# Performance work log

Measured on AMD Instinct MI355X. Metric: run time of the kernel, lower is better.

The kernel has to match this reference:

```python
import jax, jax.numpy as jnp
import numpy as np

N_NODES = 100000
N_EDGES = 1200000
D = 64          # node_feat_size
G_FEAT = 128    # graph_feat_size
N_GRAPHS = 256
N_TASKS = 1


def setup_inputs() -> dict:
    key = jax.random.key(0)
    ks = jax.random.split(key, 12)
    node_feats = jax.random.normal(ks[0], (N_NODES, D), dtype=jnp.float32)
    edge_feats = jax.random.normal(ks[1], (N_EDGES, 8), dtype=jnp.float32)
    src = jax.random.randint(ks[2], (N_EDGES,), 0, N_NODES, dtype=jnp.int64 if jax.config.read('jax_enable_x64') else jnp.int32)
    dst = jax.random.randint(ks[3], (N_EDGES,), 0, N_NODES, dtype=src.dtype)
    graph_ids = jnp.sort(jax.random.randint(ks[4], (N_NODES,), 0, N_GRAPHS, dtype=src.dtype))
    s = 1.0 / np.sqrt(D)
    W_gcn = jax.random.uniform(ks[5], (D, D), minval=-s, maxval=s, dtype=jnp.float32)
    b_gcn = jnp.zeros((D,), jnp.float32)
    W_res = jax.random.uniform(ks[6], (D, D), minval=-s, maxval=s, dtype=jnp.float32)
    b_res = jnp.zeros((D,), jnp.float32)
    W_in = jax.random.uniform(ks[7], (D, D), minval=-s, maxval=s, dtype=jnp.float32)
    b_in = jnp.zeros((D,), jnp.float32)
    W_out = jax.random.uniform(ks[8], (D, G_FEAT), minval=-s, maxval=s, dtype=jnp.float32)
    b_out = jnp.zeros((G_FEAT,), jnp.float32)
    sp = 1.0 / np.sqrt(G_FEAT)
    W_pred = jax.random.uniform(ks[9], (G_FEAT, N_TASKS), minval=-sp, maxval=sp, dtype=jnp.float32)
    b_pred = jnp.zeros((N_TASKS,), jnp.float32)
    return dict(node_feats=node_feats, edge_feats=edge_feats, src=src, dst=dst,
                graph_ids=graph_ids, W_gcn=W_gcn, b_gcn=b_gcn, W_res=W_res, b_res=b_res,
                W_in=W_in, b_in=b_in, W_out=W_out, b_out=b_out, W_pred=W_pred, b_pred=b_pred)


def reference(node_feats, edge_feats, src, dst, graph_ids,
              W_gcn, b_gcn, W_res, b_res, W_in, b_in, W_out, b_out, W_pred, b_pred):
    # --- GCNLayer (GraphConv norm='none', activation=relu, residual=True) ---
    # message passing: copy src features, sum at dst (no normalization)
    agg = jax.ops.segment_sum(node_feats[src], dst, num_segments=N_NODES)  # [N, D]
    h = jax.nn.relu(agg @ W_gcn + b_gcn)                                   # graph_conv output
    h = h + jax.nn.relu(node_feats @ W_res + b_res)                        # residual branch
    # --- MLPNodeReadout (mode='sum') ---
    h = jax.nn.relu(h @ W_in + b_in)      # [N, D]
    h = h @ W_out + b_out                 # [N, G_FEAT]
    g_feats = jax.ops.segment_sum(h, graph_ids, num_segments=N_GRAPHS)  # [G, G_FEAT]
    # --- predict ---
    out = (g_feats @ W_pred + b_pred).reshape(-1)  # [G * n_tasks]
    return out
```

## Files before the change

### kernel.cpp

```cpp
#include <hip/hip_runtime.h>

typedef __attribute__((ext_vector_type(8))) __bf16 bf16x8;
typedef __attribute__((ext_vector_type(4))) float f32x4;

union Frag { unsigned short u[8]; bf16x8 b; };

__device__ __forceinline__ unsigned short rne_bf16(float x) {
    unsigned int u = __float_as_uint(x);
    return (unsigned short)((u + 0x7fffu + ((u >> 16) & 1u)) >> 16);
}
__device__ __forceinline__ float bf16_to_f(unsigned short h) {
    return __uint_as_float(((unsigned int)h) << 16);
}

#define MFMA16 __builtin_amdgcn_mfma_f32_16x16x32_bf16
#define SBSH 10
#define SBN 1024
#define SBCAP 13056
#define BINCHUNK 4096
#define NWFRAG (3 * 2 * 2 * 4 * 64 * 8)

__global__ __launch_bounds__(256) void prepbinA_kernel(
    const float* __restrict__ nf, const int* __restrict__ src,
    const int* __restrict__ dst,
    const float* __restrict__ Wg, const float* __restrict__ Wr,
    const float* __restrict__ Wi, const float* __restrict__ Wo,
    const float* __restrict__ bo, const float* __restrict__ Wp,
    const float* __restrict__ bp,
    unsigned short* __restrict__ nfb, unsigned short* __restrict__ wfrag,
    float* __restrict__ wfold, float* __restrict__ c0, float* __restrict__ out,
    int* __restrict__ gcursor, int* __restrict__ binned,
    int nBin, int nE, int nbS, int out_size, int nNodes) {
    __shared__ int lhist[128], lbase[128], lpos[128];
    const int t = threadIdx.x;
    if ((int)blockIdx.x < nBin) {
        for (int i = t; i < nbS; i += 256) { lhist[i] = 0; lpos[i] = 0; }
        __syncthreads();
        const int e0 = blockIdx.x * BINCHUNK;
        const int e1 = min(e0 + BINCHUNK, nE);
        for (int e = e0 + t; e < e1; e += 256)
            atomicAdd(&lhist[dst[e] >> SBSH], 1);
        __syncthreads();
        for (int i = t; i < nbS; i += 256) {
            int c = lhist[i];
            lbase[i] = c ? atomicAdd(&gcursor[i], c) : 0;
        }
        __syncthreads();
        for (int e = e0 + t; e < e1; e += 256) {
            int d = dst[e];
            int sb = d >> SBSH;
            int p = atomicAdd(&lpos[sb], 1);
            int gp = lbase[sb] + p;
            if (gp < SBCAP) binned[sb * SBCAP + gp] = (src[e] << SBSH) | (d & (SBN - 1));
        }
    }
    const int tp = (int)blockIdx.x * 256 + t;
    const int nth = (int)gridDim.x * 256;
    const float4* nf4 = (const float4*)nf;
    ushort4* nfb4 = (ushort4*)nfb;
    const int nQ = nNodes * 16;
    for (int i = tp; i < nQ; i += nth) {
        float4 v = nf4[i];
        ushort4 o;
        o.x = rne_bf16(v.x); o.y = rne_bf16(v.y);
        o.z = rne_bf16(v.z); o.w = rne_bf16(v.w);
        nfb4[i] = o;
    }
    const float* Ws[3] = {Wg, Wr, Wi};
    for (int idx = tp; idx < NWFRAG; idx += nth) {
        int j = idx & 7, lane = (idx >> 3) & 63, nt = (idx >> 9) & 3;
        int kt = (idx >> 11) & 1, part = (idx >> 12) & 1, mat = idx >> 13;
        int k = kt * 32 + ((lane >> 4) << 3) + j;
        int n = nt * 16 + (lane & 15);
        float w = Ws[mat][k * 64 + n];
        unsigned short hi = rne_bf16(w);
        wfrag[idx] = (part == 0) ? hi : rne_bf16(w - bf16_to_f(hi));
    }
    if (tp < 64) {
        float s = 0.f;
        for (int j = 0; j < 128; ++j) s += Wo[tp * 128 + j] * Wp[j];
        wfold[tp] = s;
    }
    if (tp == 0) {
        float s = 0.f;
        for (int j = 0; j < 128; ++j) s += bo[j] * Wp[j];
        c0[0] = s;
    }
    if (tp < out_size) out[tp] = bp[0];
}

__global__ __launch_bounds__(1024) void segB_kernel(
    int* __restrict__ binned, const int* __restrict__ gcursor,
    int2* __restrict__ nodeTab, int nNodes) {
    __shared__ int eL[SBCAP];
    __shared__ int deg[SBN], sc[SBN], cur[SBN];
    const int b = blockIdx.x, t = threadIdx.x;
    const int cnt = min(gcursor[b], SBCAP);
    deg[t] = 0;
    __syncthreads();
    for (int i = t; i < cnt; i += 1024) {
        int p = binned[b * SBCAP + i];
        eL[i] = p;
        atomicAdd(&deg[p & (SBN - 1)], 1);
    }
    __syncthreads();
    sc[t] = deg[t];
    __syncthreads();
    #pragma unroll
    for (int s = 1; s < SBN; s <<= 1) {
        int v = (t >= s) ? sc[t - s] : 0;
        __syncthreads();
        sc[t] += v;
        __syncthreads();
    }
    {
        int excl = sc[t] - deg[t];
        cur[t] = excl;
        int node = b * SBN + t;
        if (node < nNodes) nodeTab[node] = make_int2(b * SBCAP + excl, deg[t]);
    }
    __syncthreads();
    for (int i = t; i < cnt; i += 1024) {
        int p = eL[i];
        int pos = atomicAdd(&cur[p & (SBN - 1)], 1);
        binned[b * SBCAP + pos] = p >> SBSH;
    }
}

__global__ __launch_bounds__(256) void gather_kernel(
    const unsigned short* __restrict__ nfb, const int2* __restrict__ nodeTab,
    const int* __restrict__ srcs, unsigned short* __restrict__ aggb, int nNodes) {
    int wid = blockIdx.x * 4 + (threadIdx.x >> 6);
    if (wid >= nNodes) return;
    int lane = threadIdx.x & 63;
    int half = lane >> 5;
    int cp = lane & 31;
    int2 sd = nodeTab[wid];
    int base = sd.x, d = sd.y;
    const ushort2* nfb2 = (const ushort2*)nfb;
    float ax = 0.f, ay = 0.f;
    int k = half;
    for (; k + 8 <= d; k += 8) {
        int s0 = srcs[base + k],     s1 = srcs[base + k + 2];
        int s2 = srcs[base + k + 4], s3 = srcs[base + k + 6];
        ushort2 v0 = nfb2[(long)s0 * 32 + cp];
        ushort2 v1 = nfb2[(long)s1 * 32 + cp];
        ushort2 v2 = nfb2[(long)s2 * 32 + cp];
        ushort2 v3 = nfb2[(long)s3 * 32 + cp];
        ax += (bf16_to_f(v0.x) + bf16_to_f(v1.x)) + (bf16_to_f(v2.x) + bf16_to_f(v3.x));
        ay += (bf16_to_f(v0.y) + bf16_to_f(v1.y)) + (bf16_to_f(v2.y) + bf16_to_f(v3.y));
    }
    for (; k < d; k += 2) {
        int s = srcs[base + k];
        ushort2 v = nfb2[(long)s * 32 + cp];
        ax += bf16_to_f(v.x); ay += bf16_to_f(v.y);
    }
    ax += __shfl_xor(ax, 32, 64);
    ay += __shfl_xor(ay, 32, 64);
    if (half == 0) {
        ushort2 o; o.x = rne_bf16(ax); o.y = rne_bf16(ay);
        ((ushort2*)aggb)[(long)wid * 32 + cp] = o;
    }
}

__global__ __launch_bounds__(256) void mlp_kernel(
    const unsigned short* __restrict__ aggb, const unsigned short* __restrict__ nfb,
    const int* __restrict__ gids, const unsigned short* __restrict__ wfrag,
    const float* __restrict__ bg, const float* __restrict__ br,
    const float* __restrict__ bi, const float* __restrict__ wfold,
    const float* __restrict__ c0p, float* __restrict__ out, int nTiles) {
    __shared__ float hs_all[4][32 * 68];
    const int wave = threadIdx.x >> 6, lane = threadIdx.x & 63;
    const int wid = blockIdx.x * 4 + wave;
    if (wid >= nTiles) return;
    float* hs = hs_all[wave];
    const int base = wid * 32;
    const int mrow = lane & 15, quad = lane >> 4;

    Frag aA[2][2], aN[2][2];
    #pragma unroll
    for (int rt = 0; rt < 2; ++rt) {
        const unsigned short* rowA = aggb + (long)(base + rt * 16 + mrow) * 64;
        const unsigned short* rowN = nfb  + (long)(base + rt * 16 + mrow) * 64;
        #pragma unroll
        for (int kt = 0; kt < 2; ++kt) {
            aA[rt][kt].b = *(const bf16x8*)(rowA + kt * 32 + quad * 8);
            aN[rt][kt].b = *(const bf16x8*)(rowN + kt * 32 + quad * 8);
        }
    }

    const unsigned short* wl0 = wfrag + lane * 8;
    auto WF = [&](int mat, int part, int kt, int nt) -> bf16x8 {
        return *(const bf16x8*)(wl0 + (size_t)((((mat * 2 + part) * 2 + kt) * 4 + nt) * 64) * 8);
    };

    f32x4 accA[2][4], accR[2][4];
    #pragma unroll
    for (int rt = 0; rt < 2; ++rt)
        #pragma unroll
        for (int nt = 0; nt < 4; ++nt) {
            accA[rt][nt] = (f32x4){0.f, 0.f, 0.f, 0.f};
            accR[rt][nt] = (f32x4){0.f, 0.f, 0.f, 0.f};
        }
    #pragma unroll
    for (int nt = 0; nt < 4; ++nt)
        #pragma unroll
        for (int kt = 0; kt < 2; ++kt) {
            bf16x8 gh = WF(0, 0, kt, nt), gl = WF(0, 1, kt, nt);
            bf16x8 rh = WF(1, 0, kt, nt), rl = WF(1, 1, kt, nt);
            #pragma unroll
            for (int rt = 0; rt < 2; ++rt) {
                accA[rt][nt] = MFMA16(aA[rt][kt].b, gh, accA[rt][nt], 0, 0, 0);
                accA[rt][nt] = MFMA16(aA[rt][kt].b, gl, accA[rt][nt], 0, 0, 0);
                accR[rt][nt] = MFMA16(aN[rt][kt].b, rh, accR[rt][nt], 0, 0, 0);
                accR[rt][nt] = MFMA16(aN[rt][kt].b, rl, accR[rt][nt], 0, 0, 0);
            }
        }

    #pragma unroll
    for (int nt = 0; nt < 4; ++nt) {
        float bgv = bg[nt * 16 + mrow], brv = br[nt * 16 + mrow];
        #pragma unroll
        for (int rt = 0; rt < 2; ++rt)
            #pragma unroll
            for (int r = 0; r < 4; ++r) {
                float h = fmaxf(accA[rt][nt][r] + bgv, 0.f)
                        + fmaxf(accR[rt][nt][r] + brv, 0.f);
                hs[(rt * 16 + quad * 4 + r) * 68 + nt * 16 + mrow] = h;
            }
    }
    __builtin_amdgcn_wave_barrier();

    Frag aH[2][2];
    #pragma unroll
    for (int rt = 0; rt < 2; ++rt)
        #pragma unroll
        for (int kt = 0; kt < 2; ++kt) {
            const float* hp = hs + (rt * 16 + mrow) * 68 + kt * 32 + quad * 8;
            float4 v0 = *(const float4*)hp;
            float4 v1 = *(const float4*)(hp + 4);
            aH[rt][kt].u[0] = rne_bf16(v0.x); aH[rt][kt].u[1] = rne_bf16(v0.y);
            aH[rt][kt].u[2] = rne_bf16(v0.z); aH[rt][kt].u[3] = rne_bf16(v0.w);
            aH[rt][kt].u[4] = rne_bf16(v1.x); aH[rt][kt].u[5] = rne_bf16(v1.y);
            aH[rt][kt].u[6] = rne_bf16(v1.z); aH[rt][kt].u[7] = rne_bf16(v1.w);
        }
    f32x4 accH[2][4];
    #pragma unroll
    for (int rt = 0; rt < 2; ++rt)
        #pragma unroll
        for (int nt = 0; nt < 4; ++nt)
            accH[rt][nt] = (f32x4){0.f, 0.f, 0.f, 0.f};
    #pragma unroll
    for (int nt = 0; nt < 4; ++nt)
        #pragma unroll
        for (int kt = 0; kt < 2; ++kt) {
            bf16x8 ih = WF(2, 0, kt, nt), il = WF(2, 1, kt, nt);
            #pragma unroll
            for (int rt = 0; rt < 2; ++rt) {
                accH[rt][nt] = MFMA16(aH[rt][kt].b, ih, accH[rt][nt], 0, 0, 0);
                accH[rt][nt] = MFMA16(aH[rt][kt].b, il, accH[rt][nt], 0, 0, 0);
            }
        }

    float p[2][4];
    #pragma unroll
    for (int rt = 0; rt < 2; ++rt)
        #pragma unroll
        for (int r = 0; r < 4; ++r) p[rt][r] = 0.f;
    #pragma unroll
    for (int nt = 0; nt < 4; ++nt) {
        float biv = bi[nt * 16 + mrow], wfv = wfold[nt * 16 + mrow];
        #pragma unroll
        for (int rt = 0; rt < 2; ++rt)
            #pragma unroll
            for (int r = 0; r < 4; ++r)
                p[rt][r] += fmaxf(accH[rt][nt][r] + biv, 0.f) * wfv;
    }
    #pragma unroll
    for (int m = 1; m <= 8; m <<= 1)
        #pragma unroll
        for (int rt = 0; rt < 2; ++rt)
            #pragma unroll
            for (int r = 0; r < 4; ++r)
                p[rt][r] += __shfl_xor(p[rt][r], m, 64);
    const float c0 = c0p[0];
    #pragma unroll
    for (int rt = 0; rt < 2; ++rt)
        #pragma unroll
        for (int r = 0; r < 4; ++r) p[rt][r] += c0;

    int gself = gids[base + (lane & 31)];
    int g0 = __shfl(gself, 0, 64);
    if (__all(gself == g0)) {
        float pv = 0.f;
        if (mrow == 0) {
            #pragma unroll
            for (int rt = 0; rt < 2; ++rt)
                #pragma unroll
                for (int r = 0; r < 4; ++r) pv += p[rt][r];
        }
        pv += __shfl_xor(pv, 16, 64);
        pv += __shfl_xor(pv, 32, 64);
        if (lane == 0) atomicAdd(out + g0, pv);
    } else if (mrow == 0) {
        #pragma unroll
        for (int rt = 0; rt < 2; ++rt)
            #pragma unroll
            for (int r = 0; r < 4; ++r)
                atomicAdd(out + gids[base + rt * 16 + quad * 4 + r], p[rt][r]);
    }
}

extern "C" void kernel_launch(void* const* d_in, const int* in_sizes, int n_in,
                              void* d_out, int out_size, void* d_ws, size_t ws_size,
                              hipStream_t stream) {
    const float* node_feats = (const float*)d_in[0];
    const int* src  = (const int*)d_in[2];
    const int* dst  = (const int*)d_in[3];
    const int* gids = (const int*)d_in[4];
    const float* Wg = (const float*)d_in[5];
    const float* bg = (const float*)d_in[6];
    const float* Wr = (const float*)d_in[7];
    const float* br = (const float*)d_in[8];
    const float* Wi = (const float*)d_in[9];
    const float* bi = (const float*)d_in[10];
    const float* Wo = (const float*)d_in[11];
    const float* bo = (const float*)d_in[12];
    const float* Wp = (const float*)d_in[13];
    const float* bp = (const float*)d_in[14];
    float* out = (float*)d_out;

    const int nNodes = in_sizes[0] / 64;
    const int nE = in_sizes[2];
    const int nbS = (nNodes + SBN - 1) / SBN;

    int* gcursor = (int*)d_ws;
    int* binned  = gcursor + 128;
    int2* nodeTab = (int2*)(binned + (size_t)nbS * SBCAP);
    unsigned short* nfb  = (unsigned short*)(nodeTab + nNodes);
    unsigned short* aggb = nfb + (size_t)nNodes * 64;
    unsigned short* wfrag = aggb + (size_t)nNodes * 64;
    float* wfold = (float*)(wfrag + NWFRAG);
    float* c0 = wfold + 64;

    hipMemsetAsync(gcursor, 0, 128 * sizeof(int), stream);

    const int nBin = (nE + BINCHUNK - 1) / BINCHUNK;
    prepbinA_kernel<<<nBin + 512, 256, 0, stream>>>(
        node_feats, src, dst, Wg, Wr, Wi, Wo, bo, Wp, bp,
        nfb, wfrag, wfold, c0, out, gcursor, binned,
        nBin, nE, nbS, out_size, nNodes);

    segB_kernel<<<nbS, 1024, 0, stream>>>(binned, gcursor, nodeTab, nNodes);

    gather_kernel<<<(nNodes + 3) / 4, 256, 0, stream>>>(nfb, nodeTab, binned, aggb, nNodes);

    const int nTiles = (nNodes + 31) / 32;
    mlp_kernel<<<(nTiles + 3) / 4, 256, 0, stream>>>(aggb, nfb, gids, wfrag,
        bg, br, bi, wfold, c0, out, nTiles);
}
```

Baseline: 231.7 us.

## Fuse all stages into one cooperative persistent kernel with grid syncs

```diff
diff --git a/kernel.cpp b/kernel.cpp
--- a/kernel.cpp
+++ b/kernel.cpp
@@ -1,4 +1,6 @@
 #include <hip/hip_runtime.h>
+#include <hip/hip_cooperative_groups.h>
+namespace cg = cooperative_groups;
 
 typedef __attribute__((ext_vector_type(8))) __bf16 bf16x8;
 typedef __attribute__((ext_vector_type(4))) float f32x4;
@@ -19,6 +21,309 @@
 #define SBCAP 13056
 #define BINCHUNK 4096
 #define NWFRAG (3 * 2 * 2 * 4 * 64 * 8)
+
+__global__ __launch_bounds__(256, 4) void mega_kernel(
+    const float* __restrict__ nf, const int* __restrict__ src,
+    const int* __restrict__ dst, const int* __restrict__ gids,
+    const float* __restrict__ Wg, const float* __restrict__ bg,
+    const float* __restrict__ Wr, const float* __restrict__ br,
+    const float* __restrict__ Wi, const float* __restrict__ bi,
+    const float* __restrict__ Wo, const float* __restrict__ bo,
+    const float* __restrict__ Wp, const float* __restrict__ bp,
+    int* __restrict__ gcursor, int* __restrict__ binned,
+    int* __restrict__ srcs2, int2* __restrict__ nodeTab,
+    unsigned short* __restrict__ nfb, unsigned short* __restrict__ aggb,
+    unsigned short* __restrict__ wfrag, float* __restrict__ wfold,
+    float* __restrict__ c0p, float* __restrict__ out,
+    int nBin, int nE, int nbS, int out_size, int nNodes, int nTiles)
+{
+    __shared__ float smemf[4 * 2176];
+    int* smi = (int*)smemf;
+    cg::grid_group grid = cg::this_grid();
+    const int t = threadIdx.x;
+    const int nblk = (int)gridDim.x;
+    const int wave = t >> 6, lane = t & 63;
+
+    if ((int)blockIdx.x < nBin) {
+        int* lhist = smi; int* lbase = smi + 128; int* lpos = smi + 256;
+        for (int c = blockIdx.x; c < nBin; c += nblk) {
+            for (int i = t; i < nbS; i += 256) { lhist[i] = 0; lpos[i] = 0; }
+            __syncthreads();
+            const int e0 = c * BINCHUNK;
+            const int e1 = min(e0 + BINCHUNK, nE);
+            for (int e = e0 + t; e < e1; e += 256)
+                atomicAdd(&lhist[dst[e] >> SBSH], 1);
+            __syncthreads();
+            for (int i = t; i < nbS; i += 256) {
+                int cc = lhist[i];
+                lbase[i] = cc ? atomicAdd(&gcursor[i], cc) : 0;
+            }
+            __syncthreads();
+            for (int e = e0 + t; e < e1; e += 256) {
+                int d = dst[e];
+                int sb = d >> SBSH;
+                int p = atomicAdd(&lpos[sb], 1);
+                int gp = lbase[sb] + p;
+                if (gp < SBCAP) binned[sb * SBCAP + gp] = (src[e] << SBSH) | (d & (SBN - 1));
+            }
+            __syncthreads();
+        }
+    } else {
+        const int tp = ((int)blockIdx.x - nBin) * 256 + t;
+        const int nth = (nblk - nBin) * 256;
+        const float4* nf4 = (const float4*)nf;
+        ushort4* nfb4 = (ushort4*)nfb;
+        const int nQ = nNodes * 16;
+        for (int i = tp; i < nQ; i += nth) {
+            float4 v = nf4[i];
+            ushort4 o;
+            o.x = rne_bf16(v.x); o.y = rne_bf16(v.y);
+            o.z = rne_bf16(v.z); o.w = rne_bf16(v.w);
+            nfb4[i] = o;
+        }
+        const float* Ws[3] = {Wg, Wr, Wi};
+        for (int idx = tp; idx < NWFRAG; idx += nth) {
+            int j = idx & 7, ln = (idx >> 3) & 63, nt = (idx >> 9) & 3;
+            int kt = (idx >> 11) & 1, part = (idx >> 12) & 1, mat = idx >> 13;
+            int k = kt * 32 + ((ln >> 4) << 3) + j;
+            int n = nt * 16 + (ln & 15);
+            float w = Ws[mat][k * 64 + n];
+            unsigned short hi = rne_bf16(w);
+            wfrag[idx] = (part == 0) ? hi : rne_bf16(w - bf16_to_f(hi));
+        }
+        if (tp < 64) {
+            float s = 0.f;
+            for (int j = 0; j < 128; ++j) s += Wo[tp * 128 + j] * Wp[j];
+            wfold[tp] = s;
+        }
+        if (tp == 0) {
+            float s = 0.f;
+            for (int j = 0; j < 128; ++j) s += bo[j] * Wp[j];
+            c0p[0] = s;
+        }
+        if (tp < out_size) out[tp] = bp[0];
+    }
+    __threadfence();
+    grid.sync();
+
+    {
+        int* deg = smi; int* cur = smi + 1024; int* tsum = smi + 2048;
+        for (int b = blockIdx.x; b < nbS; b += nblk) {
+            const int cnt = min(gcursor[b], SBCAP);
+            const int bb = b * SBCAP;
+            for (int j = t; j < SBN; j += 256) deg[j] = 0;
+            __syncthreads();
+            for (int i = t; i < cnt; i += 256)
+                atomicAdd(&deg[binned[bb + i] & (SBN - 1)], 1);
+            __syncthreads();
+            int d0 = deg[4 * t], d1 = deg[4 * t + 1];
+            int d2 = deg[4 * t + 2], d3 = deg[4 * t + 3];
+            int s = d0 + d1 + d2 + d3;
+            tsum[t] = s;
+            __syncthreads();
+            for (int off = 1; off < 256; off <<= 1) {
+                int v = (t >= off) ? tsum[t - off] : 0;
+                __syncthreads();
+                tsum[t] += v;
+                __syncthreads();
+            }
+            int base = tsum[t] - s;
+            int e0 = base, e1 = base + d0, e2 = e1 + d1, e3 = e2 + d2;
+            cur[4 * t] = e0; cur[4 * t + 1] = e1;
+            cur[4 * t + 2] = e2; cur[4 * t + 3] = e3;
+            int node = b * SBN + 4 * t;
+            if (node + 0 < nNodes) nodeTab[node + 0] = make_int2(bb + e0, d0);
+            if (node + 1 < nNodes) nodeTab[node + 1] = make_int2(bb + e1, d1);
+            if (node + 2 < nNodes) nodeTab[node + 2] = make_int2(bb + e2, d2);
+            if (node + 3 < nNodes) nodeTab[node + 3] = make_int2(bb + e3, d3);
+            __syncthreads();
+            for (int i = t; i < cnt; i += 256) {
+                int p = binned[bb + i];
+                int pos = atomicAdd(&cur[p & (SBN - 1)], 1);
+                srcs2[bb + pos] = p >> SBSH;
+            }
+            __syncthreads();
+        }
+    }
+    __threadfence();
+    grid.sync();
+
+    {
+        const int half = lane >> 5, cp = lane & 31;
+        const ushort2* nfb2 = (const ushort2*)nfb;
+        for (int wid = blockIdx.x * 4 + wave; wid < nNodes; wid += nblk * 4) {
+            int2 sd = nodeTab[wid];
+            int base = sd.x, d = sd.y;
+            float ax = 0.f, ay = 0.f;
+            int k = half;
+            for (; k + 8 <= d; k += 8) {
+                int s0 = srcs2[base + k],     s1 = srcs2[base + k + 2];
+                int s2 = srcs2[base + k + 4], s3 = srcs2[base + k + 6];
+                ushort2 v0 = nfb2[(long)s0 * 32 + cp];
+                ushort2 v1 = nfb2[(long)s1 * 32 + cp];
+                ushort2 v2 = nfb2[(long)s2 * 32 + cp];
+                ushort2 v3 = nfb2[(long)s3 * 32 + cp];
+                ax += (bf16_to_f(v0.x) + bf16_to_f(v1.x)) + (bf16_to_f(v2.x) + bf16_to_f(v3.x));
+                ay += (bf16_to_f(v0.y) + bf16_to_f(v1.y)) + (bf16_to_f(v2.y) + bf16_to_f(v3.y));
+            }
+            for (; k < d; k += 2) {
+                int s = srcs2[base + k];
+                ushort2 v = nfb2[(long)s * 32 + cp];
+                ax += bf16_to_f(v.x); ay += bf16_to_f(v.y);
+            }
+            ax += __shfl_xor(ax, 32, 64);
+            ay += __shfl_xor(ay, 32, 64);
+            if (half == 0) {
+                ushort2 o; o.x = rne_bf16(ax); o.y = rne_bf16(ay);
+                ((ushort2*)aggb)[(long)wid * 32 + cp] = o;
+            }
+        }
+    }
+    __threadfence();
+    grid.sync();
+
+    {
+        float* hs = smemf + wave * 2176;
+        const int mrow = lane & 15, quad = lane >> 4;
+        const unsigned short* wl0 = wfrag + lane * 8;
+        const float c0 = c0p[0];
+        for (int wid = blockIdx.x * 4 + wave; wid < nTiles; wid += nblk * 4) {
+            const int base = wid * 32;
+
+            Frag aA[2][2], aN[2][2];
+            #pragma unroll
+            for (int rt = 0; rt < 2; ++rt) {
+                const unsigned short* rowA = aggb + (long)(base + rt * 16 + mrow) * 64;
+                const unsigned short* rowN = nfb  + (long)(base + rt * 16 + mrow) * 64;
+                #pragma unroll
+                for (int kt = 0; kt < 2; ++kt) {
+                    aA[rt][kt].b = *(const bf16x8*)(rowA + kt * 32 + quad * 8);
+                    aN[rt][kt].b = *(const bf16x8*)(rowN + kt * 32 + quad * 8);
+                }
+            }
+            auto WF = [&](int mat, int part, int kt, int nt) -> bf16x8 {
+                return *(const bf16x8*)(wl0 + (size_t)((((mat * 2 + part) * 2 + kt) * 4 + nt) * 64) * 8);
+            };
+
+            f32x4 accA[2][4], accR[2][4];
+            #pragma unroll
+            for (int rt = 0; rt < 2; ++rt)
+                #pragma unroll
+                for (int nt = 0; nt < 4; ++nt) {
+                    accA[rt][nt] = (f32x4){0.f, 0.f, 0.f, 0.f};
+                    accR[rt][nt] = (f32x4){0.f, 0.f, 0.f, 0.f};
+                }
+            #pragma unroll
+            for (int nt = 0; nt < 4; ++nt)
+                #pragma unroll
+                for (int kt = 0; kt < 2; ++kt) {
+                    bf16x8 gh = WF(0, 0, kt, nt), gl = WF(0, 1, kt, nt);
+                    bf16x8 rh = WF(1, 0, kt, nt), rl = WF(1, 1, kt, nt);
+                    #pragma unroll
+                    for (int rt = 0; rt < 2; ++rt) {
+                        accA[rt][nt] = MFMA16(aA[rt][kt].b, gh, accA[rt][nt], 0, 0, 0);
+                        accA[rt][nt] = MFMA16(aA[rt][kt].b, gl, accA[rt][nt], 0, 0, 0);
+                        accR[rt][nt] = MFMA16(aN[rt][kt].b, rh, accR[rt][nt], 0, 0, 0);
+                        accR[rt][nt] = MFMA16(aN[rt][kt].b, rl, accR[rt][nt], 0, 0, 0);
+                    }
+                }
+
+            #pragma unroll
+            for (int nt = 0; nt < 4; ++nt) {
+                float bgv = bg[nt * 16 + mrow], brv = br[nt * 16 + mrow];
+                #pragma unroll
+                for (int rt = 0; rt < 2; ++rt)
+                    #pragma unroll
+                    for (int r = 0; r < 4; ++r) {
+                        float h = fmaxf(accA[rt][nt][r] + bgv, 0.f)
+                                + fmaxf(accR[rt][nt][r] + brv, 0.f);
+                        hs[(rt * 16 + quad * 4 + r) * 68 + nt * 16 + mrow] = h;
+                    }
+            }
+            __builtin_amdgcn_wave_barrier();
+
+            Frag aH[2][2];
+            #pragma unroll
+            for (int rt = 0; rt < 2; ++rt)
+                #pragma unroll
+                for (int kt = 0; kt < 2; ++kt) {
+                    const float* hp = hs + (rt * 16 + mrow) * 68 + kt * 32 + quad * 8;
+                    float4 v0 = *(const float4*)hp;
+                    float4 v1 = *(const float4*)(hp + 4);
+                    aH[rt][kt].u[0] = rne_bf16(v0.x); aH[rt][kt].u[1] = rne_bf16(v0.y);
+                    aH[rt][kt].u[2] = rne_bf16(v0.z); aH[rt][kt].u[3] = rne_bf16(v0.w);
+                    aH[rt][kt].u[4] = rne_bf16(v1.x); aH[rt][kt].u[5] = rne_bf16(v1.y);
+                    aH[rt][kt].u[6] = rne_bf16(v1.z); aH[rt][kt].u[7] = rne_bf16(v1.w);
+                }
+            __builtin_amdgcn_wave_barrier();
+            f32x4 accH[2][4];
+            #pragma unroll
+            for (int rt = 0; rt < 2; ++rt)
+                #pragma unroll
+                for (int nt = 0; nt < 4; ++nt)
+                    accH[rt][nt] = (f32x4){0.f, 0.f, 0.f, 0.f};
+            #pragma unroll
+            for (int nt = 0; nt < 4; ++nt)
+                #pragma unroll
+                for (int kt = 0; kt < 2; ++kt) {
+                    bf16x8 ih = WF(2, 0, kt, nt), il = WF(2, 1, kt, nt);
+                    #pragma unroll
+                    for (int rt = 0; rt < 2; ++rt) {
+                        accH[rt][nt] = MFMA16(aH[rt][kt].b, ih, accH[rt][nt], 0, 0, 0);
+                        accH[rt][nt] = MFMA16(aH[rt][kt].b, il, accH[rt][nt], 0, 0, 0);
+                    }
+                }
+
+            float p[2][4];
+            #pragma unroll
+            for (int rt = 0; rt < 2; ++rt)
+                #pragma unroll
+                for (int r = 0; r < 4; ++r) p[rt][r] = 0.f;
+            #pragma unroll
+            for (int nt = 0; nt < 4; ++nt) {
+                float biv = bi[nt * 16 + mrow], wfv = wfold[nt * 16 + mrow];
+                #pragma unroll
+                for (int rt = 0; rt < 2; ++rt)
+                    #pragma unroll
+                    for (int r = 0; r < 4; ++r)
+                        p[rt][r] += fmaxf(accH[rt][nt][r] + biv, 0.f) * wfv;
+            }
+            #pragma unroll
+            for (int m = 1; m <= 8; m <<= 1)
+                #pragma unroll
+                for (int rt = 0; rt < 2; ++rt)
+                    #pragma unroll
+                    for (int r = 0; r < 4; ++r)
+                        p[rt][r] += __shfl_xor(p[rt][r], m, 64);
+            #pragma unroll
+            for (int rt = 0; rt < 2; ++rt)
+                #pragma unroll
+                for (int r = 0; r < 4; ++r) p[rt][r] += c0;
+
+            int gself = gids[base + (lane & 31)];
+            int g0 = __shfl(gself, 0, 64);
+            if (__all(gself == g0)) {
+                float pv = 0.f;
+                if (mrow == 0) {
+                    #pragma unroll
+                    for (int rt = 0; rt < 2; ++rt)
+                        #pragma unroll
+                        for (int r = 0; r < 4; ++r) pv += p[rt][r];
+                }
+                pv += __shfl_xor(pv, 16, 64);
+                pv += __shfl_xor(pv, 32, 64);
+                if (lane == 0) atomicAdd(out + g0, pv);
+            } else if (mrow == 0) {
+                #pragma unroll
+                for (int rt = 0; rt < 2; ++rt)
+                    #pragma unroll
+                    for (int r = 0; r < 4; ++r)
+                        atomicAdd(out + gids[base + rt * 16 + quad * 4 + r], p[rt][r]);
+            }
+            __builtin_amdgcn_wave_barrier();
+        }
+    }
+}
 
 __global__ __launch_bounds__(256) void prepbinA_kernel(
     const float* __restrict__ nf, const int* __restrict__ src,
@@ -53,9 +358,10 @@
             int gp = lbase[sb] + p;
             if (gp < SBCAP) binned[sb * SBCAP + gp] = (src[e] << SBSH) | (d & (SBN - 1));
         }
-    }
-    const int tp = (int)blockIdx.x * 256 + t;
-    const int nth = (int)gridDim.x * 256;
+        return;
+    }
+    const int tp = ((int)blockIdx.x - nBin) * 256 + t;
+    const int nth = ((int)gridDim.x - nBin) * 256;
     const float4* nf4 = (const float4*)nf;
     ushort4* nfb4 = (ushort4*)nfb;
     const int nQ = nNodes * 16;
@@ -90,19 +396,16 @@
 }
 
 __global__ __launch_bounds__(1024) void segB_kernel(
-    int* __restrict__ binned, const int* __restrict__ gcursor,
-    int2* __restrict__ nodeTab, int nNodes) {
-    __shared__ int eL[SBCAP];
+    const int* __restrict__ binned, const int* __restrict__ gcursor,
+    int* __restrict__ srcs2, int2* __restrict__ nodeTab, int nNodes) {
     __shared__ int deg[SBN], sc[SBN], cur[SBN];
     const int b = blockIdx.x, t = threadIdx.x;
     const int cnt = min(gcursor[b], SBCAP);
+    const int bb = b * SBCAP;
     deg[t] = 0;
     __syncthreads();
-    for (int i = t; i < cnt; i += 1024) {
-        int p = binned[b * SBCAP + i];
-        eL[i] = p;
-        atomicAdd(&deg[p & (SBN - 1)], 1);
-    }
+    for (int i = t; i < cnt; i += 1024)
+        atomicAdd(&deg[binned[bb + i] & (SBN - 1)], 1);
     __syncthreads();
     sc[t] = deg[t];
     __syncthreads();
@@ -117,13 +420,13 @@
         int excl = sc[t] - deg[t];
         cur[t] = excl;
         int node = b * SBN + t;
-        if (node < nNodes) nodeTab[node] = make_int2(b * SBCAP + excl, deg[t]);
+        if (node < nNodes) nodeTab[node] = make_int2(bb + excl, deg[t]);
     }
     __syncthreads();
     for (int i = t; i < cnt; i += 1024) {
-        int p = eL[i];
+        int p = binned[bb + i];
         int pos = atomicAdd(&cur[p & (SBN - 1)], 1);
-        binned[b * SBCAP + pos] = p >> SBSH;
+        srcs2[bb + pos] = p >> SBSH;
     }
 }
 
@@ -188,12 +491,10 @@
             aN[rt][kt].b = *(const bf16x8*)(rowN + kt * 32 + quad * 8);
         }
     }
-
     const unsigned short* wl0 = wfrag + lane * 8;
     auto WF = [&](int mat, int part, int kt, int nt) -> bf16x8 {
         return *(const bf16x8*)(wl0 + (size_t)((((mat * 2 + part) * 2 + kt) * 4 + nt) * 64) * 8);
     };
-
     f32x4 accA[2][4], accR[2][4];
     #pragma unroll
     for (int rt = 0; rt < 2; ++rt)
@@ -216,7 +517,6 @@
                 accR[rt][nt] = MFMA16(aN[rt][kt].b, rl, accR[rt][nt], 0, 0, 0);
             }
         }
-
     #pragma unroll
     for (int nt = 0; nt < 4; ++nt) {
         float bgv = bg[nt * 16 + mrow], brv = br[nt * 16 + mrow];
@@ -230,7 +530,6 @@
             }
     }
     __builtin_amdgcn_wave_barrier();
-
     Frag aH[2][2];
     #pragma unroll
     for (int rt = 0; rt < 2; ++rt)
@@ -261,7 +560,6 @@
                 accH[rt][nt] = MFMA16(aH[rt][kt].b, il, accH[rt][nt], 0, 0, 0);
             }
         }
-
     float p[2][4];
     #pragma unroll
     for (int rt = 0; rt < 2; ++rt)
@@ -288,7 +586,6 @@
     for (int rt = 0; rt < 2; ++rt)
         #pragma unroll
         for (int r = 0; r < 4; ++r) p[rt][r] += c0;
-
     int gself = gids[base + (lane & 31)];
     int g0 = __shfl(gself, 0, 64);
     if (__all(gself == g0)) {
@@ -333,10 +630,13 @@
     const int nNodes = in_sizes[0] / 64;
     const int nE = in_sizes[2];
     const int nbS = (nNodes + SBN - 1) / SBN;
+    const int nBin = (nE + BINCHUNK - 1) / BINCHUNK;
+    const int nTiles = (nNodes + 31) / 32;
 
     int* gcursor = (int*)d_ws;
     int* binned  = gcursor + 128;
-    int2* nodeTab = (int2*)(binned + (size_t)nbS * SBCAP);
+    int* srcs2   = binned + (size_t)nbS * SBCAP;
+    int2* nodeTab = (int2*)(srcs2 + (size_t)nbS * SBCAP);
     unsigned short* nfb  = (unsigned short*)(nodeTab + nNodes);
     unsigned short* aggb = nfb + (size_t)nNodes * 64;
     unsigned short* wfrag = aggb + (size_t)nNodes * 64;
@@ -345,17 +645,39 @@
 
     hipMemsetAsync(gcursor, 0, 128 * sizeof(int), stream);
 
-    const int nBin = (nE + BINCHUNK - 1) / BINCHUNK;
-    prepbinA_kernel<<<nBin + 512, 256, 0, stream>>>(
-        node_feats, src, dst, Wg, Wr, Wi, Wo, bo, Wp, bp,
-        nfb, wfrag, wfold, c0, out, gcursor, binned,
-        nBin, nE, nbS, out_size, nNodes);
-
-    segB_kernel<<<nbS, 1024, 0, stream>>>(binned, gcursor, nodeTab, nNodes);
-
-    gather_kernel<<<(nNodes + 3) / 4, 256, 0, stream>>>(nfb, nodeTab, binned, aggb, nNodes);
-
-    const int nTiles = (nNodes + 31) / 32;
-    mlp_kernel<<<(nTiles + 3) / 4, 256, 0, stream>>>(aggb, nfb, gids, wfrag,
-        bg, br, bi, wfold, c0, out, nTiles);
-}
+    int dev = 0;
+    hipGetDevice(&dev);
+    int nCU = 256;
+    hipDeviceGetAttribute(&nCU, hipDeviceAttributeMultiprocessorCount, dev);
+    int occ = 0;
+    hipOccupancyMaxActiveBlocksPerMultiprocessor(&occ, mega_kernel, 256, 0);
+    if (occ < 1) occ = 1;
+    long gridL = (long)occ * nCU;
+    int grid = (int)(gridL > 2048 ? 2048 : gridL);
+
+    hipError_t err = hipErrorUnknown;
+    if (grid > nBin + 64) {
+        void* args[] = {
+            (void*)&node_feats, (void*)&src, (void*)&dst, (void*)&gids,
+            (void*)&Wg, (void*)&bg, (void*)&Wr, (void*)&br,
+            (void*)&Wi, (void*)&bi, (void*)&Wo, (void*)&bo,
+            (void*)&Wp, (void*)&bp,
+            (void*)&gcursor, (void*)&binned, (void*)&srcs2, (void*)&nodeTab,
+            (void*)&nfb, (void*)&aggb, (void*)&wfrag, (void*)&wfold,
+            (void*)&c0, (void*)&out,
+            (void*)&nBin, (void*)&nE, (void*)&nbS, (void*)&out_size,
+            (void*)&nNodes, (void*)&nTiles };
+        err = hipLaunchCooperativeKernel((void*)mega_kernel, dim3(grid), dim3(256),
+                                         args, 0, stream);
+    }
+    if (err != hipSuccess) {
+        prepbinA_kernel<<<nBin + 512, 256, 0, stream>>>(
+            node_feats, src, dst, Wg, Wr, Wi, Wo, bo, Wp, bp,
+            nfb, wfrag, wfold, c0, out, gcursor, binned,
+            nBin, nE, nbS, out_size, nNodes);
+        segB_kernel<<<nbS, 1024, 0, stream>>>(binned, gcursor, srcs2, nodeTab, nNodes);
+        gather_kernel<<<(nNodes + 3) / 4, 256, 0, stream>>>(nfb, nodeTab, srcs2, aggb, nNodes);
+        mlp_kernel<<<(nTiles + 3) / 4, 256, 0, stream>>>(aggb, nfb, gids, wfrag,
+            bg, br, bi, wfold, c0, out, nTiles);
+    }
+}
```

New measurement: 726.0 us. 213% more time.

## Locally sort binned edges in LDS before scatter and batch gather index loads

Applied to the files above, without the earlier changes.

```diff
diff --git a/kernel.cpp b/kernel.cpp
--- a/kernel.cpp
+++ b/kernel.cpp
@@ -31,31 +31,53 @@
     float* __restrict__ wfold, float* __restrict__ c0, float* __restrict__ out,
     int* __restrict__ gcursor, int* __restrict__ binned,
     int nBin, int nE, int nbS, int out_size, int nNodes) {
-    __shared__ int lhist[128], lbase[128], lpos[128];
+    __shared__ int lhist[128], lbase[128], lofs[128], lcur[128];
+    __shared__ int sortedV[BINCHUNK];
+    __shared__ int sortedA[BINCHUNK];
     const int t = threadIdx.x;
     if ((int)blockIdx.x < nBin) {
-        for (int i = t; i < nbS; i += 256) { lhist[i] = 0; lpos[i] = 0; }
-        __syncthreads();
         const int e0 = blockIdx.x * BINCHUNK;
         const int e1 = min(e0 + BINCHUNK, nE);
+        const int cnt = e1 - e0;
+        for (int i = t; i < 128; i += 256) lhist[i] = 0;
+        __syncthreads();
         for (int e = e0 + t; e < e1; e += 256)
             atomicAdd(&lhist[dst[e] >> SBSH], 1);
         __syncthreads();
-        for (int i = t; i < nbS; i += 256) {
-            int c = lhist[i];
-            lbase[i] = c ? atomicAdd(&gcursor[i], c) : 0;
+        if (t < 128) lofs[t] = lhist[t];
+        __syncthreads();
+        #pragma unroll
+        for (int s = 1; s < 128; s <<= 1) {
+            int v = 0;
+            if (t < 128 && t >= s) v = lofs[t - s];
+            __syncthreads();
+            if (t < 128) lofs[t] += v;
+            __syncthreads();
+        }
+        if (t < nbS) {
+            int c = lhist[t];
+            lbase[t] = c ? atomicAdd(&gcursor[t], c) : 0;
+            lcur[t] = lofs[t] - c;
         }
         __syncthreads();
         for (int e = e0 + t; e < e1; e += 256) {
             int d = dst[e];
             int sb = d >> SBSH;
-            int p = atomicAdd(&lpos[sb], 1);
-            int gp = lbase[sb] + p;
-            if (gp < SBCAP) binned[sb * SBCAP + gp] = (src[e] << SBSH) | (d & (SBN - 1));
-        }
-    }
-    const int tp = (int)blockIdx.x * 256 + t;
-    const int nth = (int)gridDim.x * 256;
+            int p = atomicAdd(&lcur[sb], 1);
+            sortedV[p] = (src[e] << SBSH) | (d & (SBN - 1));
+            int r = p - (lofs[sb] - lhist[sb]);
+            int gp = lbase[sb] + r;
+            sortedA[p] = (gp < SBCAP) ? (sb * SBCAP + gp) : -1;
+        }
+        __syncthreads();
+        for (int i = t; i < cnt; i += 256) {
+            int ga = sortedA[i];
+            if (ga >= 0) binned[ga] = sortedV[i];
+        }
+        return;
+    }
+    const int tp = ((int)blockIdx.x - nBin) * 256 + t;
+    const int nth = ((int)gridDim.x - nBin) * 256;
     const float4* nf4 = (const float4*)nf;
     ushort4* nfb4 = (ushort4*)nfb;
     const int nQ = nNodes * 16;
@@ -96,10 +118,11 @@
     __shared__ int deg[SBN], sc[SBN], cur[SBN];
     const int b = blockIdx.x, t = threadIdx.x;
     const int cnt = min(gcursor[b], SBCAP);
+    const int bb = b * SBCAP;
     deg[t] = 0;
     __syncthreads();
     for (int i = t; i < cnt; i += 1024) {
-        int p = binned[b * SBCAP + i];
+        int p = binned[bb + i];
         eL[i] = p;
         atomicAdd(&deg[p & (SBN - 1)], 1);
     }
@@ -117,13 +140,13 @@
         int excl = sc[t] - deg[t];
         cur[t] = excl;
         int node = b * SBN + t;
-        if (node < nNodes) nodeTab[node] = make_int2(b * SBCAP + excl, deg[t]);
+        if (node < nNodes) nodeTab[node] = make_int2(bb + excl, deg[t]);
     }
     __syncthreads();
     for (int i = t; i < cnt; i += 1024) {
         int p = eL[i];
         int pos = atomicAdd(&cur[p & (SBN - 1)], 1);
-        binned[b * SBCAP + pos] = p >> SBSH;
+        binned[bb + pos] = p >> SBSH;
     }
 }
 
@@ -139,21 +162,41 @@
     int base = sd.x, d = sd.y;
     const ushort2* nfb2 = (const ushort2*)nfb;
     float ax = 0.f, ay = 0.f;
-    int k = half;
-    for (; k + 8 <= d; k += 8) {
-        int s0 = srcs[base + k],     s1 = srcs[base + k + 2];
-        int s2 = srcs[base + k + 4], s3 = srcs[base + k + 6];
-        ushort2 v0 = nfb2[(long)s0 * 32 + cp];
-        ushort2 v1 = nfb2[(long)s1 * 32 + cp];
-        ushort2 v2 = nfb2[(long)s2 * 32 + cp];
-        ushort2 v3 = nfb2[(long)s3 * 32 + cp];
-        ax += (bf16_to_f(v0.x) + bf16_to_f(v1.x)) + (bf16_to_f(v2.x) + bf16_to_f(v3.x));
-        ay += (bf16_to_f(v0.y) + bf16_to_f(v1.y)) + (bf16_to_f(v2.y) + bf16_to_f(v3.y));
-    }
-    for (; k < d; k += 2) {
-        int s = srcs[base + k];
-        ushort2 v = nfb2[(long)s * 32 + cp];
-        ax += bf16_to_f(v.x); ay += bf16_to_f(v.y);
+    if (d > 0 && d <= 64) {
+        int myidx = srcs[base + min(lane, d - 1)];
+        int dh = (d - half + 1) >> 1;
+        for (int jb = 0; jb < dh; jb += 8) {
+            int sA[8];
+            #pragma unroll
+            for (int u = 0; u < 8; ++u) {
+                int e = 2 * (jb + u) + half;
+                sA[u] = __shfl(myidx, (e < d) ? e : (d - 1), 64);
+            }
+            ushort2 v[8];
+            #pragma unroll
+            for (int u = 0; u < 8; ++u)
+                v[u] = nfb2[(long)sA[u] * 32 + cp];
+            #pragma unroll
+            for (int u = 0; u < 8; ++u)
+                if (jb + u < dh) { ax += bf16_to_f(v[u].x); ay += bf16_to_f(v[u].y); }
+        }
+    } else if (d > 64) {
+        int k = half;
+        for (; k + 8 <= d; k += 8) {
+            int s0 = srcs[base + k],     s1 = srcs[base + k + 2];
+            int s2 = srcs[base + k + 4], s3 = srcs[base + k + 6];
+            ushort2 v0 = nfb2[(long)s0 * 32 + cp];
+            ushort2 v1 = nfb2[(long)s1 * 32 + cp];
+            ushort2 v2 = nfb2[(long)s2 * 32 + cp];
+            ushort2 v3 = nfb2[(long)s3 * 32 + cp];
+            ax += (bf16_to_f(v0.x) + bf16_to_f(v1.x)) + (bf16_to_f(v2.x) + bf16_to_f(v3.x));
+            ay += (bf16_to_f(v0.y) + bf16_to_f(v1.y)) + (bf16_to_f(v2.y) + bf16_to_f(v3.y));
+        }
+        for (; k < d; k += 2) {
+            int s = srcs[base + k];
+            ushort2 v = nfb2[(long)s * 32 + cp];
+            ax += bf16_to_f(v.x); ay += bf16_to_f(v.y);
+        }
     }
     ax += __shfl_xor(ax, 32, 64);
     ay += __shfl_xor(ay, 32, 64);
@@ -188,12 +231,10 @@
             aN[rt][kt].b = *(const bf16x8*)(rowN + kt * 32 + quad * 8);
         }
     }
-
     const unsigned short* wl0 = wfrag + lane * 8;
     auto WF = [&](int mat, int part, int kt, int nt) -> bf16x8 {
         return *(const bf16x8*)(wl0 + (size_t)((((mat * 2 + part) * 2 + kt) * 4 + nt) * 64) * 8);
     };
-
     f32x4 accA[2][4], accR[2][4];
     #pragma unroll
     for (int rt = 0; rt < 2; ++rt)
@@ -216,7 +257,6 @@
                 accR[rt][nt] = MFMA16(aN[rt][kt].b, rl, accR[rt][nt], 0, 0, 0);
             }
         }
-
     #pragma unroll
     for (int nt = 0; nt < 4; ++nt) {
         float bgv = bg[nt * 16 + mrow], brv = br[nt * 16 + mrow];
@@ -230,7 +270,6 @@
             }
     }
     __builtin_amdgcn_wave_barrier();
-
     Frag aH[2][2];
     #pragma unroll
     for (int rt = 0; rt < 2; ++rt)
@@ -261,7 +300,6 @@
                 accH[rt][nt] = MFMA16(aH[rt][kt].b, il, accH[rt][nt], 0, 0, 0);
             }
         }
-
     float p[2][4];
     #pragma unroll
     for (int rt = 0; rt < 2; ++rt)
@@ -288,7 +326,6 @@
     for (int rt = 0; rt < 2; ++rt)
         #pragma unroll
         for (int r = 0; r < 4; ++r) p[rt][r] += c0;
-
     int gself = gids[base + (lane & 31)];
     int g0 = __shfl(gself, 0, 64);
     if (__all(gself == g0)) {
@@ -333,6 +370,8 @@
     const int nNodes = in_sizes[0] / 64;
     const int nE = in_sizes[2];
     const int nbS = (nNodes + SBN - 1) / SBN;
+    const int nBin = (nE + BINCHUNK - 1) / BINCHUNK;
+    const int nTiles = (nNodes + 31) / 32;
 
     int* gcursor = (int*)d_ws;
     int* binned  = gcursor + 128;
@@ -345,7 +384,6 @@
 
     hipMemsetAsync(gcursor, 0, 128 * sizeof(int), stream);
 
-    const int nBin = (nE + BINCHUNK - 1) / BINCHUNK;
     prepbinA_kernel<<<nBin + 512, 256, 0, stream>>>(
         node_feats, src, dst, Wg, Wr, Wi, Wo, bo, Wp, bp,
         nfb, wfrag, wfold, c0, out, gcursor, binned,
@@ -355,7 +393,6 @@
 
     gather_kernel<<<(nNodes + 3) / 4, 256, 0, stream>>>(nfb, nodeTab, binned, aggb, nNodes);
 
-    const int nTiles = (nNodes + 31) / 32;
     mlp_kernel<<<(nTiles + 3) / 4, 256, 0, stream>>>(aggb, nfb, gids, wfrag,
         bg, br, bi, wfold, c0, out, nTiles);
 }
```

Result: faster. 218.9 us (-5.5%).
